# Performance work log

Measured on AMD Instinct MI355X. Metric: run time of the kernel, lower is better.

Reference implementation:

```python
import jax, jax.numpy as jnp
import numpy as np

N, M, D = 32768, 8192, 64

def setup_inputs() -> dict:
    key = jax.random.key(0)
    k1, k2, k3 = jax.random.split(key, 3)
    inputx = jax.random.normal(k1, (N, D), dtype=jnp.float32)
    y = jax.random.normal(k2, (M, D), dtype=jnp.float32)
    # psi is initialized to zeros in the module, but use random values so the
    # dual-variable subtraction actually affects the argmin/min.
    psi = jax.random.normal(k3, (M,), dtype=jnp.float32)
    return {"inputx": inputx, "y": y, "psi": psi}

def reference(inputx, y, psi):
    # cxy[i,j] = ||x_i||^2 + ||y_j||^2 - 2 <x_i, y_j>   (squared euclidean cost)
    x2 = jnp.sum(inputx * inputx, axis=1, keepdims=True)          # [N,1]
    y2 = jnp.sum(y * y, axis=1)[None, :]                          # [1,M]
    cxy = x2 + y2 - 2.0 * jnp.matmul(inputx, y.T)                 # [N,M]
    # semi-dual: mean_i min_j (c(x_i,y_j) - psi_j) + mean_j psi_j
    loss = jnp.mean(jnp.min(cxy - psi[None, :], axis=1)) + jnp.mean(psi)
    return loss
```

## Files before the change

kernel.cpp:

```cpp
#include <hip/hip_runtime.h>

#define N_ROWS 32768
#define M_COLS 8192
#define D_DIM  64
#define JC     8
#define PBLOCK 256
#define BLOCK  256
#define GROUPS 4
#define ROWS_PER_BLOCK 256
#define CHUNK  (M_COLS / JC)
#define TJ     128
#define NTILE  (CHUNK / TJ)

typedef _Float16 v8h __attribute__((ext_vector_type(8)));
typedef _Float16 v4h __attribute__((ext_vector_type(4)));
typedef float    v4f __attribute__((ext_vector_type(4)));

__global__ __launch_bounds__(PBLOCK) void prep_kernel(
    const float* __restrict__ y, const float* __restrict__ psi,
    const float* __restrict__ x, _Float16* __restrict__ yh,
    float* __restrict__ th4, _Float16* __restrict__ xh, float* __restrict__ out) {
    const int tid = threadIdx.x;
    const int bid = blockIdx.x;
    const int n = tid & 15;
    if (bid < M_COLS / 16) {
        if (bid == 0 && tid == 0) out[0] = 0.f;
        const int j = bid * 16 + (tid >> 4);
        const float4 v = *(const float4*)(y + (size_t)j * D_DIM + n * 4);
        float s = v.x * v.x + v.y * v.y + v.z * v.z + v.w * v.w;
        v4h hv = { (_Float16)v.x, (_Float16)v.y, (_Float16)v.z, (_Float16)v.w };
        *(v4h*)(yh + (size_t)j * D_DIM + n * 4) = hv;
#pragma unroll
        for (int m = 1; m < 16; m <<= 1) s += __shfl_xor(s, m, 64);
        if (n == 0) {
            const float t = 0.5f * (psi[j] - s);
            float4 t4 = { t, t, t, t };
            *(float4*)(th4 + (size_t)j * 4) = t4;
        }
    } else {
        const int i = (bid - M_COLS / 16) * 16 + (tid >> 4);
        const float4 v = *(const float4*)(x + (size_t)i * D_DIM + n * 4);
        v4h hv = { (_Float16)v.x, (_Float16)v.y, (_Float16)v.z, (_Float16)v.w };
        *(v4h*)(xh + (size_t)i * D_DIM + n * 4) = hv;
    }
}

__global__ __launch_bounds__(BLOCK) void partial_min_kernel(
    const _Float16* __restrict__ xh, const _Float16* __restrict__ yh,
    const float* __restrict__ th4, float* __restrict__ part) {
    __shared__ __align__(16) _Float16 sY[2][TJ * D_DIM];
    __shared__ __align__(16) float    sTh4[2][TJ * 4];

    const int tid  = threadIdx.x;
    const int lane = tid & 63, wave = tid >> 6;
    const int q = lane >> 4, n = lane & 15;
    const int jc    = blockIdx.y;
    const int jbase = jc * CHUNK;
    const int i_wave = blockIdx.x * ROWS_PER_BLOCK + wave * (GROUPS * 16);

    auto stage = [&](int t, int b) {
#pragma unroll
        for (int k = 0; k < 4; ++k) {
            const int sIdx = (k * 4 + wave) * 64 + lane;
            const int row  = sIdx >> 3;
            const int c    = (sIdx & 7) ^ (row & 7);
            const _Float16* g = yh + (size_t)(jbase + t * TJ + row) * D_DIM + c * 8;
            __builtin_amdgcn_global_load_lds(
                (const __attribute__((address_space(1))) void*)g,
                (__attribute__((address_space(3))) void*)(&sY[b][(size_t)(k * 4 + wave) * 512]),
                16, 0, 0);
        }
        if (wave < 2) {
            const float* gt_ = th4 + (size_t)(jbase + t * TJ + wave * 64) * 4 + lane * 4;
            __builtin_amdgcn_global_load_lds(
                (const __attribute__((address_space(1))) void*)gt_,
                (__attribute__((address_space(3))) void*)(&sTh4[b][(size_t)wave * 256]),
                16, 0, 0);
        }
    };

    stage(0, 0);

    v8h a[GROUPS][2];
#pragma unroll
    for (int g = 0; g < GROUPS; ++g) {
        const _Float16* px = xh + (size_t)(i_wave + g * 16 + n) * D_DIM + q * 8;
        a[g][0] = *(const v8h*)(px);
        a[g][1] = *(const v8h*)(px + 32);
    }

    float maxs[GROUPS][4];
#pragma unroll
    for (int g = 0; g < GROUPS; ++g)
#pragma unroll
        for (int r = 0; r < 4; ++r) maxs[g][r] = -INFINITY;

    __syncthreads();

    const int sl0 = q ^ (n & 7);

    for (int t = 0; t < NTILE; ++t) {
        const int cur = t & 1;
        if (t + 1 < NTILE) stage(t + 1, cur ^ 1);

        const _Float16* buf = &sY[cur][0];
        const float* tbuf = &sTh4[cur][0];
#pragma unroll 4
        for (int ss = 0; ss < TJ / 16; ++ss) {
            const v8h b0 = *(const v8h*)(buf + (ss * 16 + n) * 64 + sl0 * 8);
            const v8h b1 = *(const v8h*)(buf + (ss * 16 + n) * 64 + (sl0 ^ 4) * 8);
            const v4f tv4 = *(const v4f*)(tbuf + (ss * 16 + n) * 4);
#pragma unroll
            for (int g = 0; g < GROUPS; ++g) {
                v4f acc = __builtin_amdgcn_mfma_f32_16x16x32_f16(a[g][0], b0, tv4, 0, 0, 0);
                acc     = __builtin_amdgcn_mfma_f32_16x16x32_f16(a[g][1], b1, acc, 0, 0, 0);
#pragma unroll
                for (int r = 0; r < 4; ++r)
                    maxs[g][r] = fmaxf(maxs[g][r], acc[r]);
            }
        }
        __syncthreads();
    }

#pragma unroll
    for (int g = 0; g < GROUPS; ++g) {
#pragma unroll
        for (int r = 0; r < 4; ++r) {
            float v = maxs[g][r];
#pragma unroll
            for (int m = 1; m < 16; m <<= 1)
                v = fmaxf(v, __shfl_xor(v, m, 64));
            if (n == 0)
                part[(size_t)jc * N_ROWS + i_wave + g * 16 + q * 4 + r] = -2.f * v;
        }
    }
}

__global__ __launch_bounds__(PBLOCK) void reduce_kernel(
    const float* __restrict__ part, const float* __restrict__ x,
    const float* __restrict__ psi, float* __restrict__ out) {
    const int tid = threadIdx.x;
    const int gt  = blockIdx.x * PBLOCK + tid;
    float m = part[gt];
#pragma unroll
    for (int c = 1; c < JC; ++c)
        m = fminf(m, part[(size_t)c * N_ROWS + gt]);
    float s = m;
    const float4* xv = (const float4*)x;
    float x2 = 0.f;
#pragma unroll
    for (int k = 0; k < 16; ++k) {
        float4 v = xv[gt + k * 32768];
        x2 += v.x * v.x + v.y * v.y + v.z * v.z + v.w * v.w;
    }
    s = (s + x2) * (1.f / (float)N_ROWS);
    if (gt < M_COLS) s += psi[gt] * (1.f / (float)M_COLS);
    for (int off = 32; off > 0; off >>= 1) s += __shfl_down(s, off, 64);
    __shared__ float tmp[4];
    if ((tid & 63) == 0) tmp[tid >> 6] = s;
    __syncthreads();
    if (tid == 0) atomicAdd(out, tmp[0] + tmp[1] + tmp[2] + tmp[3]);
}

extern "C" void kernel_launch(void* const* d_in, const int* in_sizes, int n_in,
                              void* d_out, int out_size, void* d_ws, size_t ws_size,
                              hipStream_t stream) {
    const float* x   = (const float*)d_in[0];
    const float* y   = (const float*)d_in[1];
    const float* psi = (const float*)d_in[2];
    float* out = (float*)d_out;

    float* part = (float*)d_ws;
    float* th4  = part + (size_t)JC * N_ROWS;
    _Float16* yh = (_Float16*)(th4 + (size_t)M_COLS * 4);
    _Float16* xh = yh + (size_t)M_COLS * D_DIM;

    prep_kernel<<<(M_COLS + N_ROWS) / 16, PBLOCK, 0, stream>>>(y, psi, x, yh, th4, xh, out);
    partial_min_kernel<<<dim3(N_ROWS / ROWS_PER_BLOCK, JC), BLOCK, 0, stream>>>(xh, yh, th4, part);
    reduce_kernel<<<N_ROWS / PBLOCK, PBLOCK, 0, stream>>>(part, x, psi, out);
}
```

Measured before the change: 100.7 us.

## Switch to 32x32x16 MFMA with Y as A-operand and precompute x norms in prep

The main kernel moves from 16x16x32 to 32x32x16 MFMA tiles, with Y columns loaded from LDS as the A operand and X rows held in registers as B. Each lane now reduces a full 16-element accumulator to a single running max, which cuts the max instructions and the cross-lane shuffles in the epilogue. Theta is stored once per column instead of replicated four times, and the x squared norms move into the prep kernel so the reduce kernel no longer rereads x. In exchange each wave holds larger accumulators and more B registers, which adds register pressure under the new occupancy hint.

```diff
diff --git a/kernel.cpp b/kernel.cpp
--- a/kernel.cpp
+++ b/kernel.cpp
@@ -6,20 +6,23 @@
 #define JC     8
 #define PBLOCK 256
 #define BLOCK  256
-#define GROUPS 4
+#define RBLOCK 128
+#define GROUPS 2
 #define ROWS_PER_BLOCK 256
 #define CHUNK  (M_COLS / JC)
 #define TJ     128
 #define NTILE  (CHUNK / TJ)
 
-typedef _Float16 v8h __attribute__((ext_vector_type(8)));
-typedef _Float16 v4h __attribute__((ext_vector_type(4)));
-typedef float    v4f __attribute__((ext_vector_type(4)));
+typedef _Float16 v8h  __attribute__((ext_vector_type(8)));
+typedef _Float16 v4h  __attribute__((ext_vector_type(4)));
+typedef float    v4f  __attribute__((ext_vector_type(4)));
+typedef float    v16f __attribute__((ext_vector_type(16)));
 
 __global__ __launch_bounds__(PBLOCK) void prep_kernel(
     const float* __restrict__ y, const float* __restrict__ psi,
     const float* __restrict__ x, _Float16* __restrict__ yh,
-    float* __restrict__ th4, _Float16* __restrict__ xh, float* __restrict__ out) {
+    float* __restrict__ th, _Float16* __restrict__ xh,
+    float* __restrict__ x2, float* __restrict__ out) {
     const int tid = threadIdx.x;
     const int bid = blockIdx.x;
     const int n = tid & 15;
@@ -32,31 +35,31 @@
         *(v4h*)(yh + (size_t)j * D_DIM + n * 4) = hv;
 #pragma unroll
         for (int m = 1; m < 16; m <<= 1) s += __shfl_xor(s, m, 64);
-        if (n == 0) {
-            const float t = 0.5f * (psi[j] - s);
-            float4 t4 = { t, t, t, t };
-            *(float4*)(th4 + (size_t)j * 4) = t4;
-        }
+        if (n == 0) th[j] = 0.5f * (psi[j] - s);
     } else {
         const int i = (bid - M_COLS / 16) * 16 + (tid >> 4);
         const float4 v = *(const float4*)(x + (size_t)i * D_DIM + n * 4);
+        float s = v.x * v.x + v.y * v.y + v.z * v.z + v.w * v.w;
         v4h hv = { (_Float16)v.x, (_Float16)v.y, (_Float16)v.z, (_Float16)v.w };
         *(v4h*)(xh + (size_t)i * D_DIM + n * 4) = hv;
+#pragma unroll
+        for (int m = 1; m < 16; m <<= 1) s += __shfl_xor(s, m, 64);
+        if (n == 0) x2[i] = s;
     }
 }
 
-__global__ __launch_bounds__(BLOCK) void partial_min_kernel(
+__global__ __launch_bounds__(BLOCK, 4) void partial_min_kernel(
     const _Float16* __restrict__ xh, const _Float16* __restrict__ yh,
-    const float* __restrict__ th4, float* __restrict__ part) {
+    const float* __restrict__ th, float* __restrict__ part) {
     __shared__ __align__(16) _Float16 sY[2][TJ * D_DIM];
-    __shared__ __align__(16) float    sTh4[2][TJ * 4];
+    __shared__ __align__(16) float    sTh[2][TJ];
 
     const int tid  = threadIdx.x;
     const int lane = tid & 63, wave = tid >> 6;
-    const int q = lane >> 4, n = lane & 15;
+    const int hi = lane >> 5, r32 = lane & 31;
     const int jc    = blockIdx.y;
     const int jbase = jc * CHUNK;
-    const int i_wave = blockIdx.x * ROWS_PER_BLOCK + wave * (GROUPS * 16);
+    const int i_wave = blockIdx.x * ROWS_PER_BLOCK + wave * 64;
 
     auto stage = [&](int t, int b) {
 #pragma unroll
@@ -70,53 +73,71 @@
                 (__attribute__((address_space(3))) void*)(&sY[b][(size_t)(k * 4 + wave) * 512]),
                 16, 0, 0);
         }
-        if (wave < 2) {
-            const float* gt_ = th4 + (size_t)(jbase + t * TJ + wave * 64) * 4 + lane * 4;
+        if (wave == 0 && lane < 32) {
+            const float* gt_ = th + (size_t)(jbase + t * TJ) + lane * 4;
             __builtin_amdgcn_global_load_lds(
                 (const __attribute__((address_space(1))) void*)gt_,
-                (__attribute__((address_space(3))) void*)(&sTh4[b][(size_t)wave * 256]),
+                (__attribute__((address_space(3))) void*)(&sTh[b][0]),
                 16, 0, 0);
         }
     };
 
     stage(0, 0);
 
-    v8h a[GROUPS][2];
+    v8h b[GROUPS][4];
 #pragma unroll
     for (int g = 0; g < GROUPS; ++g) {
-        const _Float16* px = xh + (size_t)(i_wave + g * 16 + n) * D_DIM + q * 8;
-        a[g][0] = *(const v8h*)(px);
-        a[g][1] = *(const v8h*)(px + 32);
+        const _Float16* px = xh + (size_t)(i_wave + g * 32 + r32) * D_DIM + hi * 8;
+#pragma unroll
+        for (int ks = 0; ks < 4; ++ks) b[g][ks] = *(const v8h*)(px + ks * 16);
     }
 
-    float maxs[GROUPS][4];
+    float maxs[GROUPS];
 #pragma unroll
-    for (int g = 0; g < GROUPS; ++g)
-#pragma unroll
-        for (int r = 0; r < 4; ++r) maxs[g][r] = -INFINITY;
+    for (int g = 0; g < GROUPS; ++g) maxs[g] = -INFINITY;
+
+    int aoff0 = r32 * 128 + (((0 * 2 + hi) ^ (r32 & 7)) * 16);
+    int aoff1 = r32 * 128 + (((1 * 2 + hi) ^ (r32 & 7)) * 16);
+    int aoff2 = r32 * 128 + (((2 * 2 + hi) ^ (r32 & 7)) * 16);
+    int aoff3 = r32 * 128 + (((3 * 2 + hi) ^ (r32 & 7)) * 16);
 
     __syncthreads();
-
-    const int sl0 = q ^ (n & 7);
 
     for (int t = 0; t < NTILE; ++t) {
         const int cur = t & 1;
         if (t + 1 < NTILE) stage(t + 1, cur ^ 1);
 
-        const _Float16* buf = &sY[cur][0];
-        const float* tbuf = &sTh4[cur][0];
-#pragma unroll 4
-        for (int ss = 0; ss < TJ / 16; ++ss) {
-            const v8h b0 = *(const v8h*)(buf + (ss * 16 + n) * 64 + sl0 * 8);
-            const v8h b1 = *(const v8h*)(buf + (ss * 16 + n) * 64 + (sl0 ^ 4) * 8);
-            const v4f tv4 = *(const v4f*)(tbuf + (ss * 16 + n) * 4);
+        const char*  buf  = (const char*)&sY[cur][0];
+        const float* tbuf = &sTh[cur][0];
+#pragma unroll
+        for (int jb = 0; jb < TJ / 32; ++jb) {
+            const v8h a0 = *(const v8h*)(buf + jb * 4096 + aoff0);
+            const v8h a1 = *(const v8h*)(buf + jb * 4096 + aoff1);
+            const v8h a2 = *(const v8h*)(buf + jb * 4096 + aoff2);
+            const v8h a3 = *(const v8h*)(buf + jb * 4096 + aoff3);
+            const v4f tq0 = *(const v4f*)(tbuf + jb * 32 + hi * 4);
+            const v4f tq1 = *(const v4f*)(tbuf + jb * 32 + hi * 4 + 8);
+            const v4f tq2 = *(const v4f*)(tbuf + jb * 32 + hi * 4 + 16);
+            const v4f tq3 = *(const v4f*)(tbuf + jb * 32 + hi * 4 + 24);
+            v16f cin;
+#pragma unroll
+            for (int e = 0; e < 4; ++e) {
+                cin[e]      = tq0[e];
+                cin[e + 4]  = tq1[e];
+                cin[e + 8]  = tq2[e];
+                cin[e + 12] = tq3[e];
+            }
 #pragma unroll
             for (int g = 0; g < GROUPS; ++g) {
-                v4f acc = __builtin_amdgcn_mfma_f32_16x16x32_f16(a[g][0], b0, tv4, 0, 0, 0);
-                acc     = __builtin_amdgcn_mfma_f32_16x16x32_f16(a[g][1], b1, acc, 0, 0, 0);
-#pragma unroll
-                for (int r = 0; r < 4; ++r)
-                    maxs[g][r] = fmaxf(maxs[g][r], acc[r]);
+                v16f acc = __builtin_amdgcn_mfma_f32_32x32x16_f16(a0, b[g][0], cin, 0, 0, 0);
+                acc = __builtin_amdgcn_mfma_f32_32x32x16_f16(a1, b[g][1], acc, 0, 0, 0);
+                acc = __builtin_amdgcn_mfma_f32_32x32x16_f16(a2, b[g][2], acc, 0, 0, 0);
+                acc = __builtin_amdgcn_mfma_f32_32x32x16_f16(a3, b[g][3], acc, 0, 0, 0);
+                const float m0 = fmaxf(fmaxf(acc[0],  acc[1]),  fmaxf(acc[2],  acc[3]));
+                const float m1 = fmaxf(fmaxf(acc[4],  acc[5]),  fmaxf(acc[6],  acc[7]));
+                const float m2 = fmaxf(fmaxf(acc[8],  acc[9]),  fmaxf(acc[10], acc[11]));
+                const float m3 = fmaxf(fmaxf(acc[12], acc[13]), fmaxf(acc[14], acc[15]));
+                maxs[g] = fmaxf(maxs[g], fmaxf(fmaxf(m0, m1), fmaxf(m2, m3)));
             }
         }
         __syncthreads();
@@ -124,42 +145,29 @@
 
 #pragma unroll
     for (int g = 0; g < GROUPS; ++g) {
-#pragma unroll
-        for (int r = 0; r < 4; ++r) {
-            float v = maxs[g][r];
-#pragma unroll
-            for (int m = 1; m < 16; m <<= 1)
-                v = fmaxf(v, __shfl_xor(v, m, 64));
-            if (n == 0)
-                part[(size_t)jc * N_ROWS + i_wave + g * 16 + q * 4 + r] = -2.f * v;
-        }
+        float v = maxs[g];
+        v = fmaxf(v, __shfl_xor(v, 32, 64));
+        if (hi == 0)
+            part[(size_t)jc * N_ROWS + i_wave + g * 32 + r32] = -2.f * v;
     }
 }
 
-__global__ __launch_bounds__(PBLOCK) void reduce_kernel(
-    const float* __restrict__ part, const float* __restrict__ x,
+__global__ __launch_bounds__(RBLOCK) void reduce_kernel(
+    const float* __restrict__ part, const float* __restrict__ x2,
     const float* __restrict__ psi, float* __restrict__ out) {
     const int tid = threadIdx.x;
-    const int gt  = blockIdx.x * PBLOCK + tid;
+    const int gt  = blockIdx.x * RBLOCK + tid;
     float m = part[gt];
 #pragma unroll
     for (int c = 1; c < JC; ++c)
         m = fminf(m, part[(size_t)c * N_ROWS + gt]);
-    float s = m;
-    const float4* xv = (const float4*)x;
-    float x2 = 0.f;
-#pragma unroll
-    for (int k = 0; k < 16; ++k) {
-        float4 v = xv[gt + k * 32768];
-        x2 += v.x * v.x + v.y * v.y + v.z * v.z + v.w * v.w;
-    }
-    s = (s + x2) * (1.f / (float)N_ROWS);
+    float s = (m + x2[gt]) * (1.f / (float)N_ROWS);
     if (gt < M_COLS) s += psi[gt] * (1.f / (float)M_COLS);
     for (int off = 32; off > 0; off >>= 1) s += __shfl_down(s, off, 64);
-    __shared__ float tmp[4];
+    __shared__ float tmp[2];
     if ((tid & 63) == 0) tmp[tid >> 6] = s;
     __syncthreads();
-    if (tid == 0) atomicAdd(out, tmp[0] + tmp[1] + tmp[2] + tmp[3]);
+    if (tid == 0) atomicAdd(out, tmp[0] + tmp[1]);
 }
 
 extern "C" void kernel_launch(void* const* d_in, const int* in_sizes, int n_in,
@@ -171,11 +179,12 @@
     float* out = (float*)d_out;
 
     float* part = (float*)d_ws;
-    float* th4  = part + (size_t)JC * N_ROWS;
-    _Float16* yh = (_Float16*)(th4 + (size_t)M_COLS * 4);
+    float* th   = part + (size_t)JC * N_ROWS;
+    float* x2   = th + (size_t)M_COLS;
+    _Float16* yh = (_Float16*)(x2 + (size_t)N_ROWS);
     _Float16* xh = yh + (size_t)M_COLS * D_DIM;
 
-    prep_kernel<<<(M_COLS + N_ROWS) / 16, PBLOCK, 0, stream>>>(y, psi, x, yh, th4, xh, out);
-    partial_min_kernel<<<dim3(N_ROWS / ROWS_PER_BLOCK, JC), BLOCK, 0, stream>>>(xh, yh, th4, part);
-    reduce_kernel<<<N_ROWS / PBLOCK, PBLOCK, 0, stream>>>(part, x, psi, out);
+    prep_kernel<<<(M_COLS + N_ROWS) / 16, PBLOCK, 0, stream>>>(y, psi, x, yh, th, xh, x2, out);
+    partial_min_kernel<<<dim3(N_ROWS / ROWS_PER_BLOCK, JC), BLOCK, 0, stream>>>(xh, yh, th, part);
+    reduce_kernel<<<N_ROWS / RBLOCK, RBLOCK, 0, stream>>>(part, x2, psi, out);
 }
```

Measured after the change: 103.8 us. 1.03x slower.
